# Performance work log

Measured on AMD Instinct MI355X. Metric: run time of the kernel, lower is better.

The kernel has to match this reference:

```python
import jax, jax.numpy as jnp
import numpy as np
from jax import lax

N_SIN = 3

def _bn(x, g, b, m, v, eps):
    sh = [1] * x.ndim; sh[1] = -1
    r = lambda t: t.reshape(sh)
    return (x - r(m)) / jnp.sqrt(r(v) + eps) * r(g) + r(b)

def _conv2d(x, w, b, padding):
    y = lax.conv_general_dilated(x, w, (1, 1), padding,
                                 dimension_numbers=('NCHW', 'OIHW', 'NCHW'))
    return y + b[None, :, None, None]

def _causal_conv1d(x, w, b):
    k = w.shape[-1]
    y = lax.conv_general_dilated(x, w, (1,), [(k - 1, 0)],
                                 dimension_numbers=('NCH', 'OIH', 'NCH'))
    return y + b[None, :, None]

def _se(x, w1, w2):
    y = x.mean(axis=2)                                   # [B,C] global avg pool
    y = jax.nn.sigmoid(jax.nn.relu(y @ w1.T) @ w2.T)
    return x * y[:, :, None]

def _kan(x, W1, W2, B1, B2):
    # x: [B,din]; per-edge tiny MLP: sin/cos embed -> linear -> silu -> linear
    omega = (2.0 ** jnp.arange(N_SIN)).astype(x.dtype)   # [n_sin]
    ox = x[..., None] * omega                            # [B,din,n_sin]
    feat = jnp.concatenate([x[..., None], jnp.sin(ox), jnp.cos(ox)], axis=-1)  # [B,din,7]
    h = jnp.einsum('bif,ijhf->bijh', feat, W1) + B1[None]  # [B,din,dout,h]
    h = jax.nn.silu(h)
    out = jnp.einsum('bijh,ijh->bij', h, W2[:, :, 0, :]) + B2[None, :, :, 0]
    return out.sum(axis=1)                               # [B,dout]

def _lstm(x, w_ih, w_hh, b_ih, b_hh):
    B, T, E = x.shape
    H = w_hh.shape[1]
    def step(carry, xt):
        h, c = carry
        g = xt @ w_ih.T + h @ w_hh.T + (b_ih + b_hh)
        i, f, gg, o = jnp.split(g, 4, axis=-1)           # torch gate order i,f,g,o
        c = jax.nn.sigmoid(f) * c + jax.nn.sigmoid(i) * jnp.tanh(gg)
        h = jax.nn.sigmoid(o) * jnp.tanh(c)
        return (h, c), h
    init = (jnp.zeros((B, H), x.dtype), jnp.zeros((B, H), x.dtype))
    _, hs = lax.scan(step, init, jnp.swapaxes(x, 0, 1))
    return jnp.swapaxes(hs, 0, 1)                        # [B,T,H]

def _cluster(hidden):
    B, T, H = hidden.shape
    last = hidden[:, -1, :]
    hn = hidden / jnp.maximum(jnp.linalg.norm(hidden, axis=-1, keepdims=True), 1e-8)
    sim = jnp.einsum('bth,bsh->bts', hn, hn)
    sim = jnp.exp(-5.5 * (1.0 - sim))
    sim = sim * (1.0 - jnp.eye(T, dtype=sim.dtype))      # zero diagonal
    # 2-D prefix sums replace the O(T) python loop over block means
    S = jnp.cumsum(jnp.cumsum(sim, axis=1), axis=2)
    Sii = jnp.diagonal(S, axis1=1, axis2=2)[:, :T - 1]   # sum of [:i,:i]
    R = S[:, -1, :T - 1]                                 # sum of [:, :i]
    C = S[:, :T - 1, -1]                                 # sum of [:i, :]
    tot = S[:, -1, -1][:, None]
    i_f = jnp.arange(1, T, dtype=sim.dtype)
    dist = (Sii / i_f**2
            + (tot - R - C + Sii) / (T - i_f)**2
            - (C - Sii) / (i_f * (T - i_f))
            - (R - Sii) / (i_f * (T - i_f)))             # [B,T-1]
    cuts = jnp.argmax(dist, axis=1) + 1                  # [B]
    mask = (jnp.arange(T)[None, :] < cuts[:, None]).astype(hidden.dtype)
    corr = (hidden * mask[:, :, None]).sum(axis=1) / cuts[:, None].astype(hidden.dtype)
    return last, corr

def reference(x, we1, be1, bn_e1_g, bn_e1_b, bn_e1_m, bn_e1_v, we2, be2, bn_e2_g, bn_e2_b, bn_e2_m, bn_e2_v, w_ih, w_hh, b_ih, b_hh, mu_W1, mu_W2, mu_B1, mu_B2, std_W1, std_W2, std_B1, std_B2, muc_W1, muc_W2, muc_B1, muc_B2, stdc_W1, stdc_W2, stdc_B1, stdc_B2, fc_W1, fc_W2, fc_B1, fc_B2, wc1, bc1, bn1_g, bn1_b, bn1_m, bn1_v, se1_w1, se1_w2, wc2, bc2, bn2_g, bn2_b, bn2_m, bn2_v, se2_w1, se2_w2, wc3, bc3, bn3_g, bn3_b, bn3_m, bn3_v, eps1, eps2):
    gelu = lambda t: jax.nn.gelu(t, approximate=False)
    x = jnp.transpose(x, (0, 2, 1))                      # shuffle: [B,T,F]->[B,F,T]
    h2d = _conv2d(x[:, None], we1, be1, 'SAME')          # [B,4E,F,T]
    h2d = gelu(_bn(h2d, bn_e1_g, bn_e1_b, bn_e1_m, bn_e1_v, 1e-5))
    h2d = _conv2d(h2d, we2, be2, 'VALID')                # [B,E,1,T]
    h2d = gelu(_bn(h2d, bn_e2_g, bn_e2_b, bn_e2_m, bn_e2_v, 1e-5))
    x_src = jnp.transpose(h2d[:, :, 0, :], (0, 2, 1))    # [B,T,E]
    hseq = _lstm(x_src, w_ih, w_hh, b_ih, b_hh)          # [B,T,H]
    out, corr = _cluster(hseq)
    mu = _kan(corr, mu_W1, mu_W2, mu_B1, mu_B2)
    std = jax.nn.softplus(_kan(corr, std_W1, std_W2, std_B1, std_B2) - 5.0)
    z = mu + std * eps1
    x_z = jnp.concatenate([out, z], axis=1)              # [B,2H]
    mu_c = _kan(x_z, muc_W1, muc_W2, muc_B1, muc_B2)
    std_c = jax.nn.softplus(_kan(x_z, stdc_W1, stdc_W2, stdc_B1, stdc_B2) - 5.0)
    x1 = mu_c + std_c * eps2                             # dropout = identity (eval)
    x2 = jnp.transpose(x, (0, 2, 1))                     # [B,T,F]: channels = seq_len
    x2 = gelu(_bn(_causal_conv1d(x2, wc1, bc1), bn1_g, bn1_b, bn1_m, bn1_v, 1e-3))
    x2 = _se(x2, se1_w1, se1_w2)
    x2 = gelu(_bn(_causal_conv1d(x2, wc2, bc2), bn2_g, bn2_b, bn2_m, bn2_v, 1e-3))
    x2 = _se(x2, se2_w1, se2_w2)
    x2 = gelu(_bn(_causal_conv1d(x2, wc3, bc3), bn3_g, bn3_b, bn3_m, bn3_v, 1e-3))
    x2 = x2.mean(axis=2)                                 # [B,conv3_nf]
    x_all = jnp.concatenate([x1, x2], axis=1)            # [B, H+conv3_nf]
    return _kan(x_all, fc_W1, fc_W2, fc_B1, fc_B2)       # [B,num_classes]

def setup_inputs():
    key = jax.random.key(0)
    ks = iter(jax.random.split(key, 128))
    f32 = jnp.float32
    def n(shape, s=0.05):
        return s * jax.random.normal(next(ks), shape, f32)
    def bn_params(c):
        g = 1.0 + 0.05 * jax.random.normal(next(ks), (c,), f32)
        b = 0.05 * jax.random.normal(next(ks), (c,), f32)
        m = 0.05 * jax.random.normal(next(ks), (c,), f32)
        v = jax.random.uniform(next(ks), (c,), f32, 0.5, 1.5)
        return g, b, m, v
    def kan_params(din, dout, h=32, feat=1 + 2 * N_SIN):
        s = (2.0 / (feat + h)) ** 0.5
        return (n((din, dout, h, feat), s), n((din, dout, 1, h), s),
                jnp.zeros((din, dout, h), f32), jnp.zeros((din, dout, 1), f32))
    B, T, F_, E, H = 32, 256, 32, 64, 128
    inp = {}
    inp['x'] = jax.random.normal(next(ks), (B, T, F_), f32)
    inp['we1'] = n((4 * E, 1, 1, 8)); inp['be1'] = n((4 * E,))
    inp['bn_e1_g'], inp['bn_e1_b'], inp['bn_e1_m'], inp['bn_e1_v'] = bn_params(4 * E)
    inp['we2'] = n((E, 4 * E, F_, 1)); inp['be2'] = n((E,))
    inp['bn_e2_g'], inp['bn_e2_b'], inp['bn_e2_m'], inp['bn_e2_v'] = bn_params(E)
    inp['w_ih'] = n((4 * H, E)); inp['w_hh'] = n((4 * H, H))
    inp['b_ih'] = n((4 * H,)); inp['b_hh'] = n((4 * H,))
    for nm, (di, do) in [('mu', (H, H)), ('std', (H, H)), ('muc', (2 * H, H)), ('stdc', (2 * H, H)), ('fc', (2 * H, 10))]:
        w1, w2, b1, b2 = kan_params(di, do)
        inp[nm + '_W1'], inp[nm + '_W2'], inp[nm + '_B1'], inp[nm + '_B2'] = w1, w2, b1, b2
    inp['wc1'] = n((128, T, 8)); inp['bc1'] = n((128,))
    inp['bn1_g'], inp['bn1_b'], inp['bn1_m'], inp['bn1_v'] = bn_params(128)
    inp['se1_w1'] = n((8, 128)); inp['se1_w2'] = n((128, 8))
    inp['wc2'] = n((256, 128, 5)); inp['bc2'] = n((256,))
    inp['bn2_g'], inp['bn2_b'], inp['bn2_m'], inp['bn2_v'] = bn_params(256)
    inp['se2_w1'] = n((16, 256)); inp['se2_w2'] = n((256, 16))
    inp['wc3'] = n((128, 256, 3)); inp['bc3'] = n((128,))
    inp['bn3_g'], inp['bn3_b'], inp['bn3_m'], inp['bn3_v'] = bn_params(128)
    inp['eps1'] = jax.random.normal(next(ks), (B, H), f32)
    inp['eps2'] = jax.random.normal(next(ks), (B, H), f32)
    return inp
```

## Files before the change

kernel.cpp:

```cpp
#include <hip/hip_runtime.h>
#include <hip/hip_bf16.h>
#include <math.h>

typedef __hip_bfloat16 bf16;

#define DEV static __device__ __forceinline__

DEV float geluf(float x){ return 0.5f*x*(1.0f + erff(x*0.70710678118654752f)); }
DEV float sigmf(float x){ return 1.0f/(1.0f + __expf(-x)); }
DEV float softplusf(float x){ return (x > 15.f) ? x : log1pf(__expf(x)); }
DEV float tanhfast(float x){ float e = __expf(2.f*x); return fmaf(-2.f, 1.f/(e+1.f), 1.f); }

typedef __attribute__((ext_vector_type(8))) short v8s;
typedef __attribute__((ext_vector_type(4))) float v4f;
typedef _Float16 f16;
typedef f16 h2 __attribute__((ext_vector_type(2)));
typedef f16 f16x8 __attribute__((ext_vector_type(8)));
typedef unsigned u32x4 __attribute__((ext_vector_type(4)));

DEV float dot2f(h2 a, h2 b, float c){
#if __has_builtin(__builtin_amdgcn_fdot2)
  return __builtin_amdgcn_fdot2(a, b, c, false);
#else
  return fmaf((float)a.y, (float)b.y, fmaf((float)a.x, (float)b.x, c));
#endif
}

DEV h2 geth2(f16x8 v, int j){ h2 r; r.x = v[2*j]; r.y = v[2*j+1]; return r; }

enum : size_t {
  OFF_W1F   = 0,
  OFF_B1F   = 2048,
  OFF_S2E   = 2304,
  OFF_B2E   = 2368,
  OFF_WIHT  = 2432,
  OFF_BIASG = 35200,
  OFF_WHHT  = 35712,
  OFF_EPI1S = 101248,
  OFF_EPI1B = 101376,
  OFF_EPI2S = 101504,
  OFF_EPI2B = 101760,
  OFF_EPI3S = 102016,
  OFF_EPI3B = 102144,
  OFF_WE2B  = 102272,
  OFF_XSRC  = 364416,
  OFF_GX    = 888704,
  OFF_HSEQ  = 5083008,
  OFF_HN    = 6131584,
  OFF_PCOL  = 7180160,
  OFF_CCOL  = 7188352,
  OFF_CUTS  = 7196544,
  OFF_LAST  = 7196576,
  OFF_CORR  = 7200672,
  OFF_FEATA = 7204768,
  OFF_MUO   = 7233440,
  OFF_STDO  = 7237536,
  OFF_XZ    = 7241632,
  OFF_FEATB = 7249824,
  OFF_MUCO  = 7307168,
  OFF_STDCO = 7311264,
  OFF_XC1   = 7315360,
  OFF_XC2   = 7446432,
  OFF_KP    = 7708576,
  OFF_B2S   = 7741344,
  OFF_X2F   = 7839648,
  OFF_XALL  = 7843744,
  OFF_FEATC = 7851936,
  WS_FLOATS = 7909280
};

__global__ __launch_bounds__(256) void prep_kernel(
    const float* we1, const float* be1,
    const float* e1g, const float* e1b, const float* e1m, const float* e1v,
    const float* we2, const float* be2, const float* e2g, const float* e2b, const float* e2m, const float* e2v,
    const float* wih, const float* whh, const float* bih, const float* bhh,
    const float* bc1, const float* c1g, const float* c1b, const float* c1m, const float* c1v,
    const float* bc2, const float* c2g, const float* c2b, const float* c2m, const float* c2v,
    const float* bc3, const float* c3g, const float* c3b, const float* c3m, const float* c3v,
    const float* muB2, const float* sdB2, const float* mcB2, const float* scB2, const float* fcB2,
    float* ws)
{
  int idx = blockIdx.x*256 + threadIdx.x;
  if(idx < 2048){
    int o = idx>>3;
    float s = e1g[o] * rsqrtf(e1v[o] + 1e-5f);
    ws[OFF_W1F + idx] = we1[idx] * s;
  } else if(idx < 2304){
    int o = idx - 2048;
    float s = e1g[o] * rsqrtf(e1v[o] + 1e-5f);
    ws[OFF_B1F + o] = s*(be1[o] - e1m[o]) + e1b[o];
  } else if(idx < 2368){
    int e = idx - 2304;
    float s = e2g[e] * rsqrtf(e2v[e] + 1e-5f);
    ws[OFF_S2E + e] = s;
    ws[OFF_B2E + e] = s*(be2[e] - e2m[e]) + e2b[e];
  } else if(idx < 35136){
    int q = idx - 2368; int e = q>>9, g = q&511;
    ws[OFF_WIHT + q] = wih[g*64 + e];
  } else if(idx < 35648){
    int g = idx - 35136;
    ws[OFF_BIASG + g] = bih[g] + bhh[g];
  } else if(idx < 101184){
    int q = idx - 35648;
    if(q < 32768){
      int k2 = q>>9, g = q&511;
      h2 v;
      v.x = (f16)whh[g*128 + 2*k2];
      v.y = (f16)whh[g*128 + 2*k2 + 1];
      ((h2*)(ws + OFF_WHHT))[g*64 + k2] = v;
    }
  } else if(idx < 101312){
    int o = idx - 101184;
    float s = c1g[o] * rsqrtf(c1v[o] + 1e-3f);
    ws[OFF_EPI1S + o] = s;
    ws[OFF_EPI1B + o] = s*(bc1[o] - c1m[o]) + c1b[o];
  } else if(idx < 101568){
    int o = idx - 101312;
    float s = c2g[o] * rsqrtf(c2v[o] + 1e-3f);
    ws[OFF_EPI2S + o] = s;
    ws[OFF_EPI2B + o] = s*(bc2[o] - c2m[o]) + c2b[o];
  } else if(idx < 101696){
    int o = idx - 101568;
    float s = c3g[o] * rsqrtf(c3v[o] + 1e-3f);
    ws[OFF_EPI3S + o] = s;
    ws[OFF_EPI3B + o] = s*(bc3[o] - c3m[o]) + c3b[o];
  } else if(idx < 625984){
    int q = idx - 101696;
    int o = q >> 11, rem = q & 2047;
    int e = rem >> 5, f = rem & 31;
    bf16* Wr = (bf16*)(ws + OFF_WE2B);
    Wr[q] = __float2bfloat16(we2[(size_t)e*8192 + o*32 + f]);
  } else if(idx < 626112){
    int j = idx - 625984; float s = 0.f;
    for(int i=0;i<128;i++) s += muB2[i*128+j];
    ws[OFF_B2S + j] = s;
  } else if(idx < 626240){
    int j = idx - 626112; float s = 0.f;
    for(int i=0;i<128;i++) s += sdB2[i*128+j];
    ws[OFF_B2S + 128 + j] = s;
  } else if(idx < 626368){
    int j = idx - 626240; float s = 0.f;
    for(int i=0;i<256;i++) s += mcB2[i*128+j];
    ws[OFF_B2S + 256 + j] = s;
  } else if(idx < 626496){
    int j = idx - 626368; float s = 0.f;
    for(int i=0;i<256;i++) s += scB2[i*128+j];
    ws[OFF_B2S + 384 + j] = s;
  } else if(idx < 626506){
    int j = idx - 626496; float s = 0.f;
    for(int i=0;i<256;i++) s += fcB2[i*10+j];
    ws[OFF_B2S + 512 + j] = s;
  }
}

__global__ __launch_bounds__(256,1) void encoder_kernel(
    const float* __restrict__ x, const float* __restrict__ w1f, const float* __restrict__ b1f,
    const float* __restrict__ s2e, const float* __restrict__ b2e,
    const bf16* __restrict__ Wr, float* __restrict__ x_src)
{
  __shared__ float xs[39*32];
  __shared__ float w1s[2048];
  __shared__ float b1s[256];
  __shared__ __align__(16) unsigned short At[2][32*136];
  __shared__ __align__(16) unsigned short Bt[2][4*2560];

  int blk = blockIdx.x; int b = blk>>3; int t0 = (blk&7)*32;
  int tid = threadIdx.x;

  for(int i=tid;i<2048;i+=256) w1s[i] = w1f[i];
  b1s[tid] = b1f[tid];
  for(int i=tid;i<39*32;i+=256){
    int r=i>>5, f=i&31; int t=t0-3+r;
    xs[i] = (t>=0 && t<256) ? x[(b*256+t)*32+f] : 0.f;
  }
  __syncthreads();

  int f = tid & 31, tq = tid >> 5;
  int lane = tid & 63, w = tid >> 6;
  int wm = w & 1, wn = w >> 1;
  int m0 = wm*16, n0 = wn*32;
  int l15 = lane & 15, quad = lane >> 4;

  const v8s* Wv = (const v8s*)Wr;

  auto stage = [&](int cc, int buf){
    v8s bw[4];
    #pragma unroll
    for(int i=0;i<4;i++) bw[i] = Wv[cc*1024 + i*256 + tid];
    unsigned short aval[16];
    #pragma unroll
    for(int ol=0;ol<4;ol++){
      int o = cc*4 + ol;
      float wv[8];
      #pragma unroll
      for(int j=0;j<8;j++) wv[j] = w1s[o*8+j];
      float bb = b1s[o];
      #pragma unroll
      for(int i=0;i<4;i++){
        int tl = tq*4 + i;
        float c = bb;
        #pragma unroll
        for(int j=0;j<8;j++) c = fmaf(wv[j], xs[(tl+j)*32+f], c);
        aval[ol*4+i] = ((__hip_bfloat16_raw)__float2bfloat16(geluf(c))).x;
      }
    }
    #pragma unroll
    for(int ol=0;ol<4;ol++){
      #pragma unroll
      for(int i=0;i<4;i++)
        At[buf][(tq*4+i)*136 + ol*32 + f] = aval[ol*4+i];
    }
    #pragma unroll
    for(int i=0;i<4;i++){
      int j = i*256 + tid;
      int ol = j>>8, e = (j&255)>>2, f8 = j&3;
      *(v8s*)&Bt[buf][ol*2560 + e*40 + f8*8] = bw[i];
    }
  };

  stage(0, 0);
  __syncthreads();

  v4f acc0 = {0.f,0.f,0.f,0.f}, acc1 = {0.f,0.f,0.f,0.f};

  for(int c=0;c<64;c++){
    int p = c & 1, q = p ^ 1;
    if(c < 63) stage(c+1, q);
    #pragma unroll
    for(int ol=0;ol<4;ol++){
      v8s av = *(const v8s*)&At[p][(m0+l15)*136 + ol*32 + quad*8];
      v8s b0 = *(const v8s*)&Bt[p][ol*2560 + (n0+l15)*40 + quad*8];
      v8s b1 = *(const v8s*)&Bt[p][ol*2560 + (n0+16+l15)*40 + quad*8];
      acc0 = __builtin_amdgcn_mfma_f32_16x16x32_bf16(av, b0, acc0, 0, 0, 0);
      acc1 = __builtin_amdgcn_mfma_f32_16x16x32_bf16(av, b1, acc1, 0, 0, 0);
    }
    __syncthreads();
  }

  #pragma unroll
  for(int r=0;r<4;r++){
    int t = t0 + m0 + quad*4 + r;
    int e0 = n0 + l15;
    float v0 = geluf(s2e[e0]*acc0[r] + b2e[e0]);
    x_src[((size_t)(b*256+t))*64 + e0] = v0;
    int e1 = e0 + 16;
    float v1 = geluf(s2e[e1]*acc1[r] + b2e[e1]);
    x_src[((size_t)(b*256+t))*64 + e1] = v1;
  }
}

__global__ __launch_bounds__(256) void gates_kernel(
    const float* x_src, const float* wihT, const float* biasg, float* gx)
{
  __shared__ float xsh[32*64];
  int blk = blockIdx.x; int b = blk>>3, t0 = (blk&7)*32;
  int tid = threadIdx.x;
  for(int i=tid;i<2048;i+=256) xsh[i] = x_src[((size_t)b*256+t0)*64 + i];
  __syncthreads();
  int g0 = tid, g1 = tid + 256;
  float acc0[32], acc1[32];
  #pragma unroll
  for(int tt=0;tt<32;tt++){ acc0[tt]=0.f; acc1[tt]=0.f; }
  for(int e=0;e<64;e++){
    float w0 = wihT[e*512+g0], w1 = wihT[e*512+g1];
    #pragma unroll
    for(int tt=0;tt<32;tt++){
      float xv = xsh[tt*64+e];
      acc0[tt] = fmaf(xv, w0, acc0[tt]);
      acc1[tt] = fmaf(xv, w1, acc1[tt]);
    }
  }
  float bg0 = biasg[g0], bg1 = biasg[g1];
  #pragma unroll
  for(int tt=0;tt<32;tt++){
    gx[((size_t)b*256+t0+tt)*512 + g0] = acc0[tt] + bg0;
    gx[((size_t)b*256+t0+tt)*512 + g1] = acc1[tt] + bg1;
  }
}

__global__ __launch_bounds__(512)
__attribute__((amdgpu_waves_per_eu(2,2)))
void lstm_kernel(
    const float* __restrict__ gates_x, const float* __restrict__ whh16f, float* __restrict__ hseq)
{
  __shared__ __align__(16) f16 hsh[2][128];
  __shared__ float act_sh[384];
  int b = blockIdx.x, tt = threadIdx.x;
  int wave = tt >> 6, lane = tt & 63;
  int half = lane >> 5, r32 = lane & 31;
  int gA = wave*32 + r32;
  int gB = gA + 256;
  int gown = half ? gB : gA;
  bool isg = (gown >= 256) && (gown < 384);

  const u32x4* Wp = (const u32x4*)whh16f;
  u32x4 wa[8], wb[8];
  #pragma unroll
  for(int q=0;q<8;q++){
    wa[q] = Wp[gA*16 + half*8 + q];
    wb[q] = Wp[gB*16 + half*8 + q];
  }
  asm volatile("" :
    "+v"(wa[0]), "+v"(wa[1]), "+v"(wa[2]), "+v"(wa[3]),
    "+v"(wa[4]), "+v"(wa[5]), "+v"(wa[6]), "+v"(wa[7]),
    "+v"(wb[0]), "+v"(wb[1]), "+v"(wb[2]), "+v"(wb[3]),
    "+v"(wb[4]), "+v"(wb[5]), "+v"(wb[6]), "+v"(wb[7]));

  if(tt < 128) hsh[0][tt] = (f16)0.f;
  float c = 0.f;
  const float* gx = gates_x + (size_t)b*256*512;
  float na = gx[gown];
  __syncthreads();
  int p = 0;
  for(int t=0;t<256;t++){
    float a = na;
    const f16x8* hp = (const f16x8*)&hsh[p][half*64];
    f16x8 hv[8];
    #pragma unroll
    for(int k=0;k<8;k++) hv[k] = hp[k];
    if(t < 255) na = gx[(size_t)(t+1)*512 + gown];
    float sA0=0.f, sA1=0.f, sB0=0.f, sB1=0.f;
    #pragma unroll
    for(int q=0;q<8;q++){
      f16x8 W8a = __builtin_bit_cast(f16x8, wa[q]);
      f16x8 W8b = __builtin_bit_cast(f16x8, wb[q]);
      f16x8 hq = hv[q];
      sA0 = dot2f(geth2(hq,0), geth2(W8a,0), sA0);
      sA1 = dot2f(geth2(hq,1), geth2(W8a,1), sA1);
      sA0 = dot2f(geth2(hq,2), geth2(W8a,2), sA0);
      sA1 = dot2f(geth2(hq,3), geth2(W8a,3), sA1);
      sB0 = dot2f(geth2(hq,0), geth2(W8b,0), sB0);
      sB1 = dot2f(geth2(hq,1), geth2(W8b,1), sB1);
      sB0 = dot2f(geth2(hq,2), geth2(W8b,2), sB0);
      sB1 = dot2f(geth2(hq,3), geth2(W8b,3), sB1);
    }
    float pA = sA0 + sA1, pB = sB0 + sB1;
    float fullA = pA + __shfl_xor(pA, 32, 64);
    float fullB = pB + __shfl_xor(pB, 32, 64);
    a += half ? fullB : fullA;
    float arg = isg ? 2.f*a : -a;
    float e = __expf(arg);
    float qv = 1.f/(e + 1.f);
    float av = isg ? fmaf(-2.f, qv, 1.f) : qv;
    if(gown >= 128) act_sh[gown - 128] = av;
    __syncthreads();
    if(gown < 128){
      float iv = av;
      float fv = act_sh[gown];
      float gv = act_sh[128 + gown];
      float ov = act_sh[256 + gown];
      c = fv*c + iv*gv;
      float h = ov*tanhfast(c);
      hsh[p^1][gown] = (f16)h;
      hseq[((size_t)b*256+t)*128 + gown] = h;
    }
    __syncthreads();
    p ^= 1;
  }
}

__global__ __launch_bounds__(64) void hn_kernel(const float* hseq, float* hn)
{
  size_t row = blockIdx.x; int lane = threadIdx.x;
  const float* hp = hseq + row*128;
  float v0 = hp[lane], v1 = hp[lane+64];
  float ss = v0*v0 + v1*v1;
  #pragma unroll
  for(int m=1;m<64;m<<=1) ss += __shfl_xor(ss, m, 64);
  float r = 1.f / fmaxf(sqrtf(ss), 1e-8f);
  hn[row*128 + lane]      = v0*r;
  hn[row*128 + 64 + lane] = v1*r;
}

__global__ __launch_bounds__(256) void pc_kernel(const float* hn, float* pcol, float* ccol)
{
  int blk = blockIdx.x; int b = blk>>3, chunk = blk&7;
  int tid = threadIdx.x; int il = tid & 31, ts = tid >> 5;
  int i = chunk*32 + il;
  const float4* hb = (const float4*)(hn + (size_t)b*32768);
  float4 hi[32];
  #pragma unroll
  for(int r=0;r<32;r++) hi[r] = hb[(size_t)i*32 + r];
  float ps=0.f, cs=0.f;
  for(int t=ts*32; t<ts*32+32; t++){
    float dx=0.f, dy=0.f, dz=0.f, dw=0.f;
    #pragma unroll
    for(int r=0;r<32;r++){
      float4 hv = hb[(size_t)t*32 + r];
      dx = fmaf(hi[r].x, hv.x, dx);
      dy = fmaf(hi[r].y, hv.y, dy);
      dz = fmaf(hi[r].z, hv.z, dz);
      dw = fmaf(hi[r].w, hv.w, dw);
    }
    float dot = (dx+dy)+(dz+dw);
    float sim = (t==i) ? 0.f : expf(-5.5f*(1.0f - dot));
    cs += sim;
    if(t < i) ps += sim;
  }
  __shared__ float red[16][32];
  red[ts][il] = ps; red[8+ts][il] = cs;
  __syncthreads();
  if(tid < 32){
    float s=0.f;
    for(int r=0;r<8;r++) s += red[r][tid];
    pcol[b*256 + chunk*32 + tid] = s;
  } else if(tid < 64){
    int c2 = tid - 32; float s=0.f;
    for(int r=0;r<8;r++) s += red[8+r][c2];
    ccol[b*256 + chunk*32 + c2] = s;
  }
}

__global__ __launch_bounds__(256) void cutcorr_kernel(
    const float* pcol, const float* ccol, const float* hseq,
    float* last, float* corr, int* cuts)
{
  int b = blockIdx.x, tid = threadIdx.x;
  __shared__ float D[256], RC[256], dist[256];
  __shared__ int cutsh;
  if(tid == 0){
    float d=0.f, r=0.f;
    for(int i=0;i<256;i++){
      d += 2.f*pcol[b*256+i]; D[i]=d;
      r += ccol[b*256+i];     RC[i]=r;
    }
  }
  __syncthreads();
  float tot = RC[255];
  if(tid < 255){
    float Dv = D[tid], Rv = RC[tid];
    float i_f = (float)(tid+1), j_f = 256.f - i_f;
    dist[tid] = Dv/(i_f*i_f) + (tot - 2.f*Rv + Dv)/(j_f*j_f) - 2.f*(Rv - Dv)/(i_f*j_f);
  }
  __syncthreads();
  if(tid == 0){
    float best = dist[0]; int bi = 0;
    for(int i=1;i<255;i++) if(dist[i] > best){ best = dist[i]; bi = i; }
    cutsh = bi + 1; cuts[b] = cutsh;
  }
  __syncthreads();
  int cut = cutsh;
  int k = tid & 127, half = tid >> 7;
  float s = 0.f;
  for(int t=half; t<cut; t+=2) s += hseq[((size_t)b*256+t)*128 + k];
  __shared__ float partial[2][128];
  partial[half][k] = s;
  __syncthreads();
  if(tid < 128){
    corr[b*128+tid] = (partial[0][tid] + partial[1][tid]) / (float)cut;
    last[b*128+tid] = hseq[((size_t)b*256+255)*128 + tid];
  }
}

__global__ __launch_bounds__(256) void feat_kernel(const float* xin, float* feat, int n)
{
  int idx = blockIdx.x*256 + threadIdx.x;
  if(idx >= n) return;
  float xv = xin[idx];
  float* fp = feat + (size_t)idx*7;
  fp[0]=xv;
  fp[1]=sinf(xv); fp[2]=sinf(2.f*xv); fp[3]=sinf(4.f*xv);
  fp[4]=cosf(xv); fp[5]=cosf(2.f*xv); fp[6]=cosf(4.f*xv);
}

__global__ __launch_bounds__(256) void kanp_kernel(
    const float* __restrict__ feat, const float* __restrict__ W1,
    const float* __restrict__ B1, const float* __restrict__ W2,
    int din, int dout, float* __restrict__ partial)
{
  __shared__ float feat_s[32*225];
  __shared__ float red[8][32];
  int j = blockIdx.x, ic = blockIdx.y;
  int i0 = ic*32;
  int tid = threadIdx.x;
  int b = tid & 31, hg = tid >> 5;
  for(int q=tid; q<1792; q+=256){
    int br = q/56, qq = q - br*56;
    float4 v = *(const float4*)(feat + ((size_t)br*din + i0)*7 + qq*4);
    float* d = &feat_s[br*225 + qq*4];
    d[0]=v.x; d[1]=v.y; d[2]=v.z; d[3]=v.w;
  }
  __syncthreads();
  float acc = 0.f;
  const float* fb = &feat_s[b*225];
  for(int ii=0; ii<32; ii++){
    int i = i0 + ii;
    size_t hbase = ((size_t)i*dout + j)*32 + hg*4;
    const float4* w1p = (const float4*)(W1 + ((size_t)i*dout + j)*224 + hg*28);
    float w1a[28];
    #pragma unroll
    for(int q=0;q<7;q++) *(float4*)&w1a[q*4] = w1p[q];
    float4 b1v = *(const float4*)(B1 + hbase);
    float4 w2v = *(const float4*)(W2 + hbase);
    float f[7];
    #pragma unroll
    for(int q=0;q<7;q++) f[q] = fb[ii*7+q];
    float b1a[4] = {b1v.x, b1v.y, b1v.z, b1v.w};
    float w2a[4] = {w2v.x, w2v.y, w2v.z, w2v.w};
    #pragma unroll
    for(int hh=0;hh<4;hh++){
      float hv = b1a[hh];
      #pragma unroll
      for(int q=0;q<7;q++) hv = fmaf(f[q], w1a[hh*7+q], hv);
      float sv = hv / (1.f + __expf(-hv));
      acc = fmaf(sv, w2a[hh], acc);
    }
  }
  red[hg][b] = acc;
  __syncthreads();
  if(tid < 32){
    float s = 0.f;
    #pragma unroll
    for(int q=0;q<8;q++) s += red[q][tid];
    partial[((size_t)ic*32 + tid)*dout + j] = s;
  }
}

__global__ __launch_bounds__(256) void kanr_kernel(
    const float* __restrict__ partial, const float* __restrict__ b2s,
    int NI, int dout, float* __restrict__ outp)
{
  int idx = blockIdx.x*256 + threadIdx.x;
  if(idx >= 32*dout) return;
  int b = idx / dout, j = idx - b*dout;
  float s = b2s[j];
  for(int ic=0; ic<NI; ic++) s += partial[((size_t)ic*32 + b)*dout + j];
  outp[idx] = s;
}

__global__ __launch_bounds__(256) void zmix_kernel(
    const float* muo, const float* stdo, const float* eps1, const float* last, float* xz)
{
  int idx = blockIdx.x*256 + threadIdx.x;
  if(idx >= 4096) return;
  int b = idx >> 7, k = idx & 127;
  float z = muo[idx] + softplusf(stdo[idx] - 5.f)*eps1[idx];
  xz[b*256 + k]       = last[idx];
  xz[b*256 + 128 + k] = z;
}

__global__ __launch_bounds__(256) void xall_kernel(
    const float* muco, const float* stdco, const float* eps2, const float* x2f, float* xa)
{
  int idx = blockIdx.x*256 + threadIdx.x;
  if(idx >= 4096) return;
  int b = idx >> 7, k = idx & 127;
  xa[b*256 + k]       = muco[idx] + softplusf(stdco[idx] - 5.f)*eps2[idx];
  xa[b*256 + 128 + k] = x2f[idx];
}

template<int CIN, int K, int COUT, int NCH, int LG>
__global__ __launch_bounds__(COUT*LG, 1) void convp_kernel(
    const float* __restrict__ xin, const float* __restrict__ w, float* __restrict__ part)
{
  constexpr int L = 32/LG;
  constexpr int CCH = CIN/NCH;
  __shared__ float xsh[CCH*32];
  int b = blockIdx.x, ch = blockIdx.y;
  int tid = threadIdx.x;
  for(int i=tid; i<CCH*32; i+=COUT*LG) xsh[i] = xin[((size_t)b*CIN + ch*CCH)*32 + i];
  __syncthreads();
  int o = tid / LG, lh = tid % LG;
  int l0 = lh*L;
  float acc[L];
  #pragma unroll
  for(int j=0;j<L;j++) acc[j]=0.f;
  const float* wrow = w + ((size_t)o*CIN + ch*CCH)*K;
  for(int c=0;c<CCH;c++){
    float wv[K];
    #pragma unroll
    for(int k=0;k<K;k++) wv[k] = wrow[c*K + k];
    float xr[L+K-1];
    #pragma unroll
    for(int i=0;i<L+K-1;i++){
      int li = l0 - (K-1) + i;
      xr[i] = (li>=0) ? xsh[c*32+li] : 0.f;
    }
    #pragma unroll
    for(int j=0;j<L;j++){
      #pragma unroll
      for(int k=0;k<K;k++) acc[j] = fmaf(xr[j+k], wv[k], acc[j]);
    }
  }
  float* pp = part + (((size_t)ch*32 + b)*COUT + o)*32 + l0;
  #pragma unroll
  for(int j=0;j<L;j++) pp[j] = acc[j];
}

template<int C, int R, int NP>
__global__ __launch_bounds__(C,1) void sef_kernel(
    const float* __restrict__ part, const float* __restrict__ epi_s, const float* __restrict__ epi_b,
    const float* __restrict__ w1, const float* __restrict__ w2, float* __restrict__ out)
{
  __shared__ float mean[C];
  __shared__ float y1[R];
  int b = blockIdx.x, c = threadIdx.x;
  float g[32];
  #pragma unroll
  for(int l=0;l<32;l++) g[l]=0.f;
  for(int p=0;p<NP;p++){
    const float* pp = part + (((size_t)p*32 + b)*C + c)*32;
    #pragma unroll
    for(int l=0;l<32;l++) g[l] += pp[l];
  }
  float s = epi_s[c], bb = epi_b[c];
  float m = 0.f;
  #pragma unroll
  for(int l=0;l<32;l++){ g[l] = geluf(s*g[l]+bb); m += g[l]; }
  mean[c] = m*(1.f/32.f);
  __syncthreads();
  if(c < R){
    float t=0.f;
    for(int k=0;k<C;k++) t = fmaf(mean[k], w1[c*C+k], t);
    y1[c] = fmaxf(t,0.f);
  }
  __syncthreads();
  float t=0.f;
  #pragma unroll
  for(int k=0;k<R;k++) t = fmaf(y1[k], w2[c*R+k], t);
  float sc = sigmf(t);
  float* op = out + ((size_t)b*C + c)*32;
  #pragma unroll
  for(int l=0;l<32;l++) op[l] = g[l]*sc;
}

__global__ __launch_bounds__(128,1) void mean3f_kernel(
    const float* __restrict__ part, const float* __restrict__ epi_s, const float* __restrict__ epi_b,
    float* __restrict__ x2f)
{
  int b = blockIdx.x, c = threadIdx.x;
  float g[32];
  #pragma unroll
  for(int l=0;l<32;l++) g[l]=0.f;
  for(int p=0;p<8;p++){
    const float* pp = part + (((size_t)p*32 + b)*128 + c)*32;
    #pragma unroll
    for(int l=0;l<32;l++) g[l] += pp[l];
  }
  float s = epi_s[c], bb = epi_b[c];
  float m = 0.f;
  #pragma unroll
  for(int l=0;l<32;l++) m += geluf(s*g[l]+bb);
  x2f[b*128 + c] = m*(1.f/32.f);
}

extern "C" void kernel_launch(void* const* d_in, const int* in_sizes, int n_in,
                              void* d_out, int out_size, void* d_ws, size_t ws_size,
                              hipStream_t stream)
{
  const float* x    = (const float*)d_in[0];
  const float* we1  = (const float*)d_in[1];
  const float* be1  = (const float*)d_in[2];
  const float* e1g  = (const float*)d_in[3];
  const float* e1b  = (const float*)d_in[4];
  const float* e1m  = (const float*)d_in[5];
  const float* e1v  = (const float*)d_in[6];
  const float* we2  = (const float*)d_in[7];
  const float* be2  = (const float*)d_in[8];
  const float* e2g  = (const float*)d_in[9];
  const float* e2b  = (const float*)d_in[10];
  const float* e2m  = (const float*)d_in[11];
  const float* e2v  = (const float*)d_in[12];
  const float* wih  = (const float*)d_in[13];
  const float* whh  = (const float*)d_in[14];
  const float* bih  = (const float*)d_in[15];
  const float* bhh  = (const float*)d_in[16];
  const float* muW1 = (const float*)d_in[17];
  const float* muW2 = (const float*)d_in[18];
  const float* muB1 = (const float*)d_in[19];
  const float* muB2 = (const float*)d_in[20];
  const float* sdW1 = (const float*)d_in[21];
  const float* sdW2 = (const float*)d_in[22];
  const float* sdB1 = (const float*)d_in[23];
  const float* sdB2 = (const float*)d_in[24];
  const float* mcW1 = (const float*)d_in[25];
  const float* mcW2 = (const float*)d_in[26];
  const float* mcB1 = (const float*)d_in[27];
  const float* mcB2 = (const float*)d_in[28];
  const float* scW1 = (const float*)d_in[29];
  const float* scW2 = (const float*)d_in[30];
  const float* scB1 = (const float*)d_in[31];
  const float* scB2 = (const float*)d_in[32];
  const float* fcW1 = (const float*)d_in[33];
  const float* fcW2 = (const float*)d_in[34];
  const float* fcB1 = (const float*)d_in[35];
  const float* fcB2 = (const float*)d_in[36];
  const float* wc1  = (const float*)d_in[37];
  const float* bc1  = (const float*)d_in[38];
  const float* c1g  = (const float*)d_in[39];
  const float* c1b  = (const float*)d_in[40];
  const float* c1m  = (const float*)d_in[41];
  const float* c1v  = (const float*)d_in[42];
  const float* se1w1= (const float*)d_in[43];
  const float* se1w2= (const float*)d_in[44];
  const float* wc2  = (const float*)d_in[45];
  const float* bc2  = (const float*)d_in[46];
  const float* c2g  = (const float*)d_in[47];
  const float* c2b  = (const float*)d_in[48];
  const float* c2m  = (const float*)d_in[49];
  const float* c2v  = (const float*)d_in[50];
  const float* se2w1= (const float*)d_in[51];
  const float* se2w2= (const float*)d_in[52];
  const float* wc3  = (const float*)d_in[53];
  const float* bc3  = (const float*)d_in[54];
  const float* c3g  = (const float*)d_in[55];
  const float* c3b  = (const float*)d_in[56];
  const float* c3m  = (const float*)d_in[57];
  const float* c3v  = (const float*)d_in[58];
  const float* eps1 = (const float*)d_in[59];
  const float* eps2 = (const float*)d_in[60];

  float* ws = (float*)d_ws;
  float* part = ws + OFF_GX;
  float* kp   = ws + OFF_KP;
  float* b2s  = ws + OFF_B2S;

  prep_kernel<<<2448, 256, 0, stream>>>(we1, be1, e1g,e1b,e1m,e1v,
      we2, be2,e2g,e2b,e2m,e2v, wih,whh,bih,bhh,
      bc1,c1g,c1b,c1m,c1v, bc2,c2g,c2b,c2m,c2v, bc3,c3g,c3b,c3m,c3v,
      muB2, sdB2, mcB2, scB2, fcB2, ws);

  encoder_kernel<<<256, 256, 0, stream>>>(x, ws+OFF_W1F, ws+OFF_B1F,
      ws+OFF_S2E, ws+OFF_B2E, (const bf16*)(ws+OFF_WE2B), ws+OFF_XSRC);

  gates_kernel<<<256, 256, 0, stream>>>(ws+OFF_XSRC, ws+OFF_WIHT, ws+OFF_BIASG, ws+OFF_GX);
  lstm_kernel<<<32, 512, 0, stream>>>(ws+OFF_GX, ws+OFF_WHHT, ws+OFF_HSEQ);

  hn_kernel<<<8192, 64, 0, stream>>>(ws+OFF_HSEQ, ws+OFF_HN);
  pc_kernel<<<256, 256, 0, stream>>>(ws+OFF_HN, ws+OFF_PCOL, ws+OFF_CCOL);
  cutcorr_kernel<<<32, 256, 0, stream>>>(ws+OFF_PCOL, ws+OFF_CCOL, ws+OFF_HSEQ,
      ws+OFF_LAST, ws+OFF_CORR, (int*)(ws+OFF_CUTS));

  feat_kernel<<<16, 256, 0, stream>>>(ws+OFF_CORR, ws+OFF_FEATA, 4096);
  kanp_kernel<<<dim3(128,4), 256, 0, stream>>>(ws+OFF_FEATA, muW1, muB1, muW2, 128, 128, kp);
  kanr_kernel<<<16, 256, 0, stream>>>(kp, b2s+0, 4, 128, ws+OFF_MUO);
  kanp_kernel<<<dim3(128,4), 256, 0, stream>>>(ws+OFF_FEATA, sdW1, sdB1, sdW2, 128, 128, kp);
  kanr_kernel<<<16, 256, 0, stream>>>(kp, b2s+128, 4, 128, ws+OFF_STDO);
  zmix_kernel<<<16, 256, 0, stream>>>(ws+OFF_MUO, ws+OFF_STDO, eps1, ws+OFF_LAST, ws+OFF_XZ);
  feat_kernel<<<32, 256, 0, stream>>>(ws+OFF_XZ, ws+OFF_FEATB, 8192);
  kanp_kernel<<<dim3(128,8), 256, 0, stream>>>(ws+OFF_FEATB, mcW1, mcB1, mcW2, 256, 128, kp);
  kanr_kernel<<<16, 256, 0, stream>>>(kp, b2s+256, 8, 128, ws+OFF_MUCO);
  kanp_kernel<<<dim3(128,8), 256, 0, stream>>>(ws+OFF_FEATB, scW1, scB1, scW2, 256, 128, kp);
  kanr_kernel<<<16, 256, 0, stream>>>(kp, b2s+384, 8, 128, ws+OFF_STDCO);

  convp_kernel<256,8,128,8,2><<<dim3(32,8), 256, 0, stream>>>(x, wc1, part);
  sef_kernel<128,8,8><<<32, 128, 0, stream>>>(part, ws+OFF_EPI1S, ws+OFF_EPI1B, se1w1, se1w2, ws+OFF_XC1);
  convp_kernel<128,5,256,4,1><<<dim3(32,4), 256, 0, stream>>>(ws+OFF_XC1, wc2, part);
  sef_kernel<256,16,4><<<32, 256, 0, stream>>>(part, ws+OFF_EPI2S, ws+OFF_EPI2B, se2w1, se2w2, ws+OFF_XC2);
  convp_kernel<256,3,128,8,2><<<dim3(32,8), 256, 0, stream>>>(ws+OFF_XC2, wc3, part);
  mean3f_kernel<<<32, 128, 0, stream>>>(part, ws+OFF_EPI3S, ws+OFF_EPI3B, ws+OFF_X2F);

  xall_kernel<<<16, 256, 0, stream>>>(ws+OFF_MUCO, ws+OFF_STDCO, eps2, ws+OFF_X2F, ws+OFF_XALL);
  feat_kernel<<<32, 256, 0, stream>>>(ws+OFF_XALL, ws+OFF_FEATC, 8192);
  kanp_kernel<<<dim3(10,8), 256, 0, stream>>>(ws+OFF_FEATC, fcW1, fcB1, fcW2, 256, 10, kp);
  kanr_kernel<<<2, 256, 0, stream>>>(kp, b2s+512, 8, 10, (float*)d_out);
}
```

Baseline: 970.9 us.

## Remap LSTM gate ownership so gate exchange uses shuffles and one barrier per step

Gate rows are reassigned so the four gates (i,f,g,o) of each hidden unit land in lanes of a single wave. They are then combined with a lane shuffle instead of a shared-memory act buffer, which removes one of the two block barriers per timestep. The time loop is also unrolled by two with double-buffer indices fixed at compile time, and the input-gate prefetch now runs two steps ahead. Each lane now computes two activations, one of them duplicated across lanes, and the cell state is replicated across lanes, which adds some redundant transcendental work.

```diff
diff --git a/kernel.cpp b/kernel.cpp
--- a/kernel.cpp
+++ b/kernel.cpp
@@ -278,20 +278,63 @@
   }
 }
 
+#define LSTM_STEP(AG, BG, PR, PW, T)                                         \
+  {                                                                          \
+    const f16x8* hp = (const f16x8*)&hsh[PR][half*64];                       \
+    f16x8 hvv[8];                                                            \
+    _Pragma("unroll")                                                        \
+    for(int q=0;q<8;q++) hvv[q] = hp[q];                                     \
+    float sA0=0.f,sA1=0.f,sB0=0.f,sB1=0.f;                                   \
+    _Pragma("unroll")                                                        \
+    for(int q=0;q<8;q++){                                                    \
+      f16x8 W8a = __builtin_bit_cast(f16x8, wa[q]);                          \
+      f16x8 W8b = __builtin_bit_cast(f16x8, wb[q]);                          \
+      f16x8 hq = hvv[q];                                                     \
+      sA0 = dot2f(geth2(hq,0), geth2(W8a,0), sA0);                           \
+      sA1 = dot2f(geth2(hq,1), geth2(W8a,1), sA1);                           \
+      sA0 = dot2f(geth2(hq,2), geth2(W8a,2), sA0);                           \
+      sA1 = dot2f(geth2(hq,3), geth2(W8a,3), sA1);                           \
+      sB0 = dot2f(geth2(hq,0), geth2(W8b,0), sB0);                           \
+      sB1 = dot2f(geth2(hq,1), geth2(W8b,1), sB1);                           \
+      sB0 = dot2f(geth2(hq,2), geth2(W8b,2), sB0);                           \
+      sB1 = dot2f(geth2(hq,3), geth2(W8b,3), sB1);                           \
+    }                                                                        \
+    float pA = sA0+sA1, pB = sB0+sB1;                                        \
+    float fullA = (AG) + pA + __shfl_xor(pA, 32, 64);                        \
+    float fullB = (BG) + pB + __shfl_xor(pB, 32, 64);                        \
+    float argA = dup ? 2.f*fullA : -fullA;                                   \
+    float eA = __expf(argA);                                                 \
+    float qA = 1.f/(eA + 1.f);                                               \
+    float vA = dup ? fmaf(-2.f, qA, 1.f) : qA;      \
+    float vB = 1.f/(1.f + __expf(-fullB));          \
+    float oA = __shfl_xor(vA, 16, 64);                                       \
+    float oB = __shfl_xor(vB, 16, 64);                                       \
+    float iv = dup ? oA : vA;                                                \
+    float gv = dup ? vA : oA;                                                \
+    float fv = dup ? oB : vB;                                                \
+    float ov = dup ? vB : oB;                                                \
+    c = fmaf(fv, c, iv*gv);                                                  \
+    float h = ov*tanhfast(c);                                                \
+    if(lane < 16){                                                           \
+      hsh[PW][n] = (f16)h;                                                   \
+      hseq[((size_t)b*256+(T))*128 + n] = h;                                 \
+    }                                                                        \
+    __syncthreads();                                                         \
+  }
+
 __global__ __launch_bounds__(512)
 __attribute__((amdgpu_waves_per_eu(2,2)))
 void lstm_kernel(
     const float* __restrict__ gates_x, const float* __restrict__ whh16f, float* __restrict__ hseq)
 {
   __shared__ __align__(16) f16 hsh[2][128];
-  __shared__ float act_sh[384];
   int b = blockIdx.x, tt = threadIdx.x;
   int wave = tt >> 6, lane = tt & 63;
-  int half = lane >> 5, r32 = lane & 31;
-  int gA = wave*32 + r32;
-  int gB = gA + 256;
-  int gown = half ? gB : gA;
-  bool isg = (gown >= 256) && (gown < 384);
+  int n = wave*16 + (lane & 15);
+  int dup  = (lane >> 4) & 1;
+  int half = lane >> 5;
+  int gA = dup ? (256 + n) : n;
+  int gB = gA + 128;
 
   const u32x4* Wp = (const u32x4*)whh16f;
   u32x4 wa[8], wb[8];
@@ -309,53 +352,16 @@
   if(tt < 128) hsh[0][tt] = (f16)0.f;
   float c = 0.f;
   const float* gx = gates_x + (size_t)b*256*512;
-  float na = gx[gown];
-  __syncthreads();
-  int p = 0;
-  for(int t=0;t<256;t++){
-    float a = na;
-    const f16x8* hp = (const f16x8*)&hsh[p][half*64];
-    f16x8 hv[8];
-    #pragma unroll
-    for(int k=0;k<8;k++) hv[k] = hp[k];
-    if(t < 255) na = gx[(size_t)(t+1)*512 + gown];
-    float sA0=0.f, sA1=0.f, sB0=0.f, sB1=0.f;
-    #pragma unroll
-    for(int q=0;q<8;q++){
-      f16x8 W8a = __builtin_bit_cast(f16x8, wa[q]);
-      f16x8 W8b = __builtin_bit_cast(f16x8, wb[q]);
-      f16x8 hq = hv[q];
-      sA0 = dot2f(geth2(hq,0), geth2(W8a,0), sA0);
-      sA1 = dot2f(geth2(hq,1), geth2(W8a,1), sA1);
-      sA0 = dot2f(geth2(hq,2), geth2(W8a,2), sA0);
-      sA1 = dot2f(geth2(hq,3), geth2(W8a,3), sA1);
-      sB0 = dot2f(geth2(hq,0), geth2(W8b,0), sB0);
-      sB1 = dot2f(geth2(hq,1), geth2(W8b,1), sB1);
-      sB0 = dot2f(geth2(hq,2), geth2(W8b,2), sB0);
-      sB1 = dot2f(geth2(hq,3), geth2(W8b,3), sB1);
-    }
-    float pA = sA0 + sA1, pB = sB0 + sB1;
-    float fullA = pA + __shfl_xor(pA, 32, 64);
-    float fullB = pB + __shfl_xor(pB, 32, 64);
-    a += half ? fullB : fullA;
-    float arg = isg ? 2.f*a : -a;
-    float e = __expf(arg);
-    float qv = 1.f/(e + 1.f);
-    float av = isg ? fmaf(-2.f, qv, 1.f) : qv;
-    if(gown >= 128) act_sh[gown - 128] = av;
-    __syncthreads();
-    if(gown < 128){
-      float iv = av;
-      float fv = act_sh[gown];
-      float gv = act_sh[128 + gown];
-      float ov = act_sh[256 + gown];
-      c = fv*c + iv*gv;
-      float h = ov*tanhfast(c);
-      hsh[p^1][gown] = (f16)h;
-      hseq[((size_t)b*256+t)*128 + gown] = h;
-    }
-    __syncthreads();
-    p ^= 1;
+  float aC = gx[gA],       bC = gx[gB];
+  float aN = gx[512 + gA], bN = gx[512 + gB];
+  __syncthreads();
+  for(int t=0; t<256; t+=2){
+    float a2=0.f, b2=0.f, a3=0.f, b3=0.f;
+    if(t+2 < 256){ a2 = gx[(size_t)(t+2)*512 + gA]; b2 = gx[(size_t)(t+2)*512 + gB]; }
+    LSTM_STEP(aC, bC, 0, 1, t);
+    if(t+3 < 256){ a3 = gx[(size_t)(t+3)*512 + gA]; b3 = gx[(size_t)(t+3)*512 + gB]; }
+    LSTM_STEP(aN, bN, 1, 0, t+1);
+    aC=a2; bC=b2; aN=a3; bN=b3;
   }
 }
 
```

Result: no change. 975.7 us (+0.5%).
